# Performance work log

Measured on AMD Instinct MI355X. Metric: run time of the kernel, lower is better.

## Reference

```python
import jax, jax.numpy as jnp
import numpy as np
import math

DIM = 384
NUM_HEADS = 12
WS = 8  # window_size


def setup_inputs() -> dict:
    key = jax.random.key(0)
    k1, k2, k3 = jax.random.split(key, 3)
    B, N, C = 16, 4096, DIM
    x = jax.random.normal(k1, (B, N, C), dtype=jnp.float32)
    W_qkv = jax.random.normal(k2, (C, 3 * C), dtype=jnp.float32) * 0.02
    b_qkv = jnp.zeros((3 * C,), dtype=jnp.float32)
    W_proj = jax.random.normal(k3, (C, C), dtype=jnp.float32) * 0.02
    return {"x": x, "W_qkv": W_qkv, "b_qkv": b_qkv, "W_proj": W_proj}


def window_attention(x, W_qkv, b_qkv, W_proj):
    B, N, C = x.shape
    H = W = int(math.isqrt(N))
    nh = NUM_HEADS
    hd = C // nh
    scale = hd ** (-0.5)
    ws = WS
    pad_h = (ws - H % ws) % ws
    pad_w = (ws - W % ws) % ws
    xg = x.reshape(B, H, W, C)
    if pad_h or pad_w:
        xg = jnp.pad(xg, ((0, 0), (0, pad_h), (0, pad_w), (0, 0)))
    Hp, Wp = H + pad_h, W + pad_w
    nH, nW = Hp // ws, Wp // ws
    # partition into windows: [B, nWin, ws*ws, C]
    xw = xg.reshape(B, nH, ws, nW, ws, C).transpose(0, 1, 3, 2, 4, 5)
    xw = xw.reshape(B, nH * nW, ws * ws, C)
    # qkv projection
    qkv = xw @ W_qkv + b_qkv  # [B, nWin, ws2, 3C]
    qkv = qkv.reshape(B, nH * nW, ws * ws, 3, nh, hd)
    q = qkv[..., 0, :, :].transpose(0, 1, 3, 2, 4)  # [B, nWin, nh, ws2, hd]
    k = qkv[..., 1, :, :].transpose(0, 1, 3, 2, 4)
    v = qkv[..., 2, :, :].transpose(0, 1, 3, 2, 4)
    attn = jnp.einsum('bwhqd,bwhkd->bwhqk', q, k) * scale
    attn = jax.nn.softmax(attn, axis=-1)
    out = jnp.einsum('bwhqk,bwhkd->bwhqd', attn, v)
    out = out.transpose(0, 1, 3, 2, 4).reshape(B, nH * nW, ws * ws, C)
    out = out @ W_proj
    # un-partition windows
    out = out.reshape(B, nH, nW, ws, ws, C).transpose(0, 1, 3, 2, 4, 5)
    out = out.reshape(B, Hp, Wp, C)
    if pad_h or pad_w:
        out = out[:, :H, :W, :]
    return out.reshape(B, H * W, C)


def reference(x, W_qkv, b_qkv, W_proj):
    return window_attention(x, W_qkv, b_qkv, W_proj)
```

## Files before the change

### kernel.cpp

```cpp
#include <hip/hip_runtime.h>
#include <hip/hip_bf16.h>


typedef _Float16 f16;
typedef f16 f16x8 __attribute__((ext_vector_type(8)));
typedef f16 f16x4 __attribute__((ext_vector_type(4)));
typedef float f32x4 __attribute__((ext_vector_type(4)));

#define MFMA_F16(a, b, c) __builtin_amdgcn_mfma_f32_16x16x32_f16((a), (b), (c), 0, 0, 0)

#define AS_G __attribute__((address_space(1)))
#define AS_L __attribute__((address_space(3)))
#define GLOAD_LDS16(gp, lp) \
  __builtin_amdgcn_global_load_lds((const AS_G void*)(gp), (AS_L void*)(lp), 16, 0, 0)
#define WAITVM_(N) asm volatile("s_waitcnt vmcnt(" #N ")" ::: "memory")
#define WAITVM(N) WAITVM_(N)

namespace {
constexpr int kC = 384;
constexpr int kNTok = 4096;
constexpr float kScale = 0.17677669529663687f;
constexpr int kWqPackChunks = 72 * 12 * 64;
constexpr int kWpPackChunks = 24 * 12 * 64;
constexpr size_t kWqPackBytes = (size_t)kWqPackChunks * 16;
constexpr size_t kWpPackBytes = (size_t)kWpPackChunks * 16;
constexpr size_t kQkvWsBytes = (size_t)65536 * 1152 * 2;
constexpr size_t kWsNeed = kWqPackBytes + kWpPackBytes + kQkvWsBytes;
constexpr int kQkvPackChunksFb = 6 * 12 * 12 * 64;
}


__global__ void prep_weights_split(const float* __restrict__ Wqkv,
                                   const float* __restrict__ Wproj,
                                   f16* __restrict__ wq_pack,
                                   f16* __restrict__ wp_pack) {
  int i = blockIdx.x * 256 + threadIdx.x;
  if (i < kWqPackChunks) {
    int lane = i & 63;
    int chunk = i >> 6;
    int ks = chunk % 12;
    int t = chunk / 12;
    int l15 = lane & 15, g = lane >> 4;
    int n3 = t * 16 + l15;
    int k0 = ks * 32 + g * 8;
    f16x8 v;
    #pragma unroll
    for (int j = 0; j < 8; ++j)
      v[j] = (f16)Wqkv[(size_t)(k0 + j) * (3 * kC) + n3];
    *reinterpret_cast<f16x8*>(wq_pack + (size_t)i * 8) = v;
  } else if (i < kWqPackChunks + kWpPackChunks) {
    int p = i - kWqPackChunks;
    int lane = p & 63;
    int chunk = p >> 6;
    int ks = chunk % 12;
    int t = chunk / 12;
    int l15 = lane & 15, g = lane >> 4;
    int n = t * 16 + l15;
    int k0 = ks * 32 + g * 8;
    f16x8 v;
    #pragma unroll
    for (int j = 0; j < 8; ++j)
      v[j] = (f16)Wproj[(size_t)(k0 + j) * kC + n];
    *reinterpret_cast<f16x8*>(wp_pack + (size_t)p * 8) = v;
  }
}

__global__ void prep_x(const float* __restrict__ x, f16* __restrict__ xw) {
  int c = blockIdx.x * 256 + threadIdx.x;
  int lane = c & 63;
  int t = c >> 6;
  int ks = t % 12;
  int mb = t / 12;
  int l15 = lane & 15, g = lane >> 4;
  int m = mb * 16 + l15;
  int b = m >> 12;
  int win = (m >> 6) & 63;
  int tok = m & 63;
  int n = ((win >> 3) * 8 + (tok >> 3)) * 64 + (win & 7) * 8 + (tok & 7);
  const float* src = x + ((size_t)(b << 12) + n) * kC + ks * 32 + g * 8;
  float4 v0 = *reinterpret_cast<const float4*>(src);
  float4 v1 = *reinterpret_cast<const float4*>(src + 4);
  f16x8 h = {(f16)v0.x, (f16)v0.y, (f16)v0.z, (f16)v0.w,
             (f16)v1.x, (f16)v1.y, (f16)v1.z, (f16)v1.w};
  *reinterpret_cast<f16x8*>(xw + (size_t)c * 8) = h;
}

__global__ __launch_bounds__(256, 3) void qkv_gemm2(
    const f16* __restrict__ xw, const float* __restrict__ b_qkv,
    const f16* __restrict__ wq_pack, f16* __restrict__ qkv_ws) {
  __shared__ alignas(1024) char smem[49152];

  const int tid = threadIdx.x;
  const int wid = tid >> 6;
  const int lane = tid & 63;
  const int g = lane >> 4;
  const int l15 = lane & 15;
  const int wm = wid >> 1;
  const int wn = wid & 1;

  int bid = blockIdx.x;
  int wg = (bid & 7) * 576 + (bid >> 3);
  int m_grp = wg / 9;
  int n_grp = wg - m_grp * 9;
  const int mb0 = m_grp * 8;
  const int nb0 = n_grp * 8;

  #define STAGE(KS, BUF)                                                     \
    do {                                                                     \
      const f16* ga0 = xw + (((size_t)(mb0 + wid) * 12 + (KS)) * 64 + lane) * 8;     \
      const f16* ga1 = xw + (((size_t)(mb0 + 4 + wid) * 12 + (KS)) * 64 + lane) * 8; \
      const f16* gb0 =                                                       \
          wq_pack + (((size_t)(nb0 + wid) * 12 + (KS)) * 64 + lane) * 8;     \
      const f16* gb1 =                                                       \
          wq_pack + (((size_t)(nb0 + 4 + wid) * 12 + (KS)) * 64 + lane) * 8; \
      char* la = smem + (BUF) * 16384 + wid * 1024;                          \
      char* lb = smem + (BUF) * 16384 + 8192 + wid * 1024;                   \
      GLOAD_LDS16(ga0, la);                                                  \
      GLOAD_LDS16(ga1, la + 4096);                                           \
      GLOAD_LDS16(gb0, lb);                                                  \
      GLOAD_LDS16(gb1, lb + 4096);                                           \
    } while (0)

  f32x4 acc[4][4];
  #pragma unroll
  for (int mt = 0; mt < 4; ++mt)
    #pragma unroll
    for (int nt = 0; nt < 4; ++nt) acc[mt][nt] = {0.f, 0.f, 0.f, 0.f};

  STAGE(0, 0);
  STAGE(1, 1);
  STAGE(2, 2);
  WAITVM(8);
  __builtin_amdgcn_sched_barrier(0);
  __builtin_amdgcn_s_barrier();

  #define KITER(T, ENDVM)                                                    \
    do {                                                                     \
      constexpr int buf = (T) % 3;                                           \
      f16x8 af[4], bf[4];                                                    \
      _Pragma("unroll") for (int mt = 0; mt < 4; ++mt) af[mt] =              \
          *reinterpret_cast<const f16x8*>(smem + buf * 16384 +               \
                                          (wm * 4 + mt) * 1024 + lane * 16); \
      _Pragma("unroll") for (int nt = 0; nt < 4; ++nt) bf[nt] =              \
          *reinterpret_cast<const f16x8*>(smem + buf * 16384 + 8192 +        \
                                          (wn * 4 + nt) * 1024 + lane * 16); \
      asm volatile("s_waitcnt lgkmcnt(0)" ::: "memory");                     \
      __builtin_amdgcn_sched_barrier(0);                                     \
      __builtin_amdgcn_s_barrier();                                          \
      if ((T) < 9) {                                                         \
        STAGE((T) + 3, buf);                                                 \
      }                                                                      \
      __builtin_amdgcn_s_setprio(1);                                         \
      _Pragma("unroll") for (int mt = 0; mt < 4; ++mt)                       \
          _Pragma("unroll") for (int nt = 0; nt < 4; ++nt) acc[mt][nt] =     \
          MFMA_F16(af[mt], bf[nt], acc[mt][nt]);                             \
      __builtin_amdgcn_s_setprio(0);                                         \
      WAITVM(ENDVM);                                                         \
      __builtin_amdgcn_sched_barrier(0);                                     \
      __builtin_amdgcn_s_barrier();                                          \
    } while (0)

  KITER(0, 8);
  KITER(1, 8);
  KITER(2, 8);
  KITER(3, 8);
  KITER(4, 8);
  KITER(5, 8);
  KITER(6, 8);
  KITER(7, 8);
  KITER(8, 8);
  KITER(9, 4);
  KITER(10, 0);
  KITER(11, 0);
  #undef KITER
  #undef STAGE

  f16* eo = (f16*)smem;
  #pragma unroll
  for (int nt = 0; nt < 4; ++nt) {
    int col128 = wn * 64 + nt * 16 + l15;
    float bias = b_qkv[n_grp * 128 + col128];
    int hsec_loc = wn * 2 + (nt >> 1);
    int d = col128 & 31;
    int sec = (n_grp * 4 + hsec_loc) / 12;
    int base = (wm * 4 + hsec_loc) * 2048;
    #pragma unroll
    for (int mt = 0; mt < 4; ++mt) {
      #pragma unroll
      for (int j = 0; j < 4; ++j) {
        int tok = mt * 16 + g * 4 + j;
        f16 hv = (f16)(acc[mt][nt][j] + bias);
        if (sec == 2)
          eo[base + d * 64 + (tok ^ ((d & 7) << 3))] = hv;
        else
          eo[base + tok * 32 + d] = hv;
      }
    }
  }
  __syncthreads();
  #pragma unroll
  for (int i = 0; i < 8; ++i) {
    int u = tid + i * 256;
    int win_loc = u >> 10;
    int cbl = (u >> 8) & 3;
    int inner = u & 255;
    int cb = n_grp * 4 + cbl;
    int h = cb % 12;
    int sec = cb / 12;
    size_t dst = ((size_t)(m_grp * 2 + win_loc) * 36 + h * 3 + sec) * 2048 +
                 (size_t)inner * 8;
    f16x8 hv;
    if (sec == 2) {
      int d = inner >> 3;
      int t0 = inner & 7;
      hv = *reinterpret_cast<const f16x8*>(
          eo + (win_loc * 4 + cbl) * 2048 + d * 64 + ((t0 * 8) ^ ((d & 7) << 3)));
    } else {
      hv = *reinterpret_cast<const f16x8*>(eo + (size_t)u * 8);
    }
    *reinterpret_cast<f16x8*>(qkv_ws + dst) = hv;
  }
}

__global__ __launch_bounds__(768, 2) void attn_proj2(
    const f16* __restrict__ qkv_ws, const f16* __restrict__ wp_pack,
    float* __restrict__ out) {
  __shared__ alignas(16) f16 ao[64][392];
  __shared__ alignas(16) f16 p_s[12][16][68];

  const int tid = threadIdx.x;
  const int wid = tid >> 6;
  const int lane = tid & 63;
  const int g = lane >> 4;
  const int l15 = lane & 15;

  int blk = (int)blockIdx.x;
  blk = (blk & 7) * 128 + (blk >> 3);
  const int b = blk >> 6;
  const int win = blk & 63;
  const int wh = win >> 3;
  const int ww = win & 7;

  const f32x4 zero4 = {0.f, 0.f, 0.f, 0.f};
  const f16* hb = qkv_ws + ((size_t)(b * 64 + win) * 36 + wid * 3) * 2048;

  f16x8 qf[4], kf[4], vf[2][2];
  #pragma unroll
  for (int mt = 0; mt < 4; ++mt)
    qf[mt] = *reinterpret_cast<const f16x8*>(hb + (mt * 16 + l15) * 32 + g * 8);
  #pragma unroll
  for (int nt = 0; nt < 4; ++nt)
    kf[nt] = *reinterpret_cast<const f16x8*>(hb + 2048 + (nt * 16 + l15) * 32 + g * 8);
  #pragma unroll
  for (int ntd = 0; ntd < 2; ++ntd)
    #pragma unroll
    for (int ks = 0; ks < 2; ++ks)
      vf[ntd][ks] = *reinterpret_cast<const f16x8*>(
          hb + 4096 + (ntd * 16 + l15) * 64 + ks * 32 + g * 8);

  f32x4 sacc[4][4];
  #pragma unroll
  for (int mt = 0; mt < 4; ++mt)
    #pragma unroll
    for (int nt = 0; nt < 4; ++nt) sacc[mt][nt] = zero4;
  #pragma unroll
  for (int mt = 0; mt < 4; ++mt)
    #pragma unroll
    for (int nt = 0; nt < 4; ++nt)
      sacc[mt][nt] = MFMA_F16(qf[mt], kf[nt], sacc[mt][nt]);

  f32x4 oacc[4][2];
  #pragma unroll
  for (int mt = 0; mt < 4; ++mt) {
    oacc[mt][0] = zero4;
    oacc[mt][1] = zero4;
  }
  #pragma unroll
  for (int mt = 0; mt < 4; ++mt) {
    float pv[4][4];
    #pragma unroll
    for (int j = 0; j < 4; ++j) {
      float m = -1e30f;
      #pragma unroll
      for (int nt = 0; nt < 4; ++nt) {
        pv[nt][j] = sacc[mt][nt][j] * kScale;
        m = fmaxf(m, pv[nt][j]);
      }
      m = fmaxf(m, __shfl_xor(m, 1));
      m = fmaxf(m, __shfl_xor(m, 2));
      m = fmaxf(m, __shfl_xor(m, 4));
      m = fmaxf(m, __shfl_xor(m, 8));
      float s = 0.f;
      #pragma unroll
      for (int nt = 0; nt < 4; ++nt) {
        pv[nt][j] = __expf(pv[nt][j] - m);
        s += pv[nt][j];
      }
      s += __shfl_xor(s, 1);
      s += __shfl_xor(s, 2);
      s += __shfl_xor(s, 4);
      s += __shfl_xor(s, 8);
      float inv = 1.0f / s;
      #pragma unroll
      for (int nt = 0; nt < 4; ++nt)
        p_s[wid][g * 4 + j][nt * 16 + l15] = (f16)(pv[nt][j] * inv);
    }
    #pragma unroll
    for (int ks = 0; ks < 2; ++ks) {
      f16x8 pa =
          *reinterpret_cast<const f16x8*>(&p_s[wid][l15][ks * 32 + g * 8]);
      #pragma unroll
      for (int ntd = 0; ntd < 2; ++ntd)
        oacc[mt][ntd] = MFMA_F16(pa, vf[ntd][ks], oacc[mt][ntd]);
    }
    #pragma unroll
    for (int ntd = 0; ntd < 2; ++ntd)
      #pragma unroll
      for (int j = 0; j < 4; ++j)
        ao[mt * 16 + g * 4 + j][wid * 32 + ntd * 16 + l15] =
            (f16)oacc[mt][ntd][j];
  }
  __syncthreads();

  f32x4 pacc[4][2];
  #pragma unroll
  for (int mt = 0; mt < 4; ++mt) {
    pacc[mt][0] = zero4;
    pacc[mt][1] = zero4;
  }
  const f16* pptr[2];
  #pragma unroll
  for (int nt = 0; nt < 2; ++nt) {
    int t = wid * 2 + nt;
    pptr[nt] = wp_pack + ((size_t)(t * 12) * 64 + lane) * 8;
  }
  f16x8 pbf[2][2];
  #pragma unroll
  for (int nt = 0; nt < 2; ++nt)
    pbf[0][nt] = *reinterpret_cast<const f16x8*>(pptr[nt]);

  #pragma unroll
  for (int ks = 0; ks < 12; ++ks) {
    const int cur = ks & 1;
    if (ks < 11) {
      #pragma unroll
      for (int nt = 0; nt < 2; ++nt)
        pbf[cur ^ 1][nt] =
            *reinterpret_cast<const f16x8*>(pptr[nt] + (ks + 1) * 512);
    }
    f16x8 paf[4];
    #pragma unroll
    for (int mt = 0; mt < 4; ++mt)
      paf[mt] = *reinterpret_cast<const f16x8*>(
          &ao[mt * 16 + l15][ks * 32 + g * 8]);
    #pragma unroll
    for (int mt = 0; mt < 4; ++mt)
      #pragma unroll
      for (int nt = 0; nt < 2; ++nt)
        pacc[mt][nt] = MFMA_F16(paf[mt], pbf[cur][nt], pacc[mt][nt]);
  }

  const size_t outbase = (size_t)b * kNTok * kC;
  #pragma unroll
  for (int mt = 0; mt < 4; ++mt) {
    #pragma unroll
    for (int j = 0; j < 4; ++j) {
      int r = mt * 16 + g * 4 + j;
      int n = (wh * 8 + (r >> 3)) * 64 + ww * 8 + (r & 7);
      float* orow = out + outbase + (size_t)n * kC + wid * 32;
      #pragma unroll
      for (int nt = 0; nt < 2; ++nt) orow[nt * 16 + l15] = pacc[mt][nt][j];
    }
  }
}


__global__ void prep_weights_fb(const float* __restrict__ Wqkv,
                                const float* __restrict__ Wproj,
                                f16* __restrict__ wq_pack,
                                f16* __restrict__ wp_pack) {
  int i = blockIdx.x * 256 + threadIdx.x;
  if (i < kQkvPackChunksFb) {
    int lane = i & 63;
    int chunk = i >> 6;
    int ks = chunk % 12;
    int t = (chunk / 12) % 12;
    int hp = chunk / 144;
    int l15 = lane & 15, g = lane >> 4;
    int base = t * 16;
    int hh = base / 96;
    int cc = base - hh * 96;
    int sec = cc >> 5;
    int dbhi = cc & 31;
    int n3 = sec * kC + (2 * hp + hh) * 32 + dbhi + l15;
    int k0 = ks * 32 + g * 8;
    f16x8 v;
    #pragma unroll
    for (int j = 0; j < 8; ++j)
      v[j] = (f16)Wqkv[(size_t)(k0 + j) * (3 * kC) + n3];
    *reinterpret_cast<f16x8*>(wq_pack + (size_t)i * 8) = v;
  } else if (i < kQkvPackChunksFb + kWpPackChunks) {
    int p = i - kQkvPackChunksFb;
    int lane = p & 63;
    int chunk = p >> 6;
    int ks = chunk % 12;
    int t = chunk / 12;
    int l15 = lane & 15, g = lane >> 4;
    int n = t * 16 + l15;
    int k0 = ks * 32 + g * 8;
    f16x8 v;
    #pragma unroll
    for (int j = 0; j < 8; ++j)
      v[j] = (f16)Wproj[(size_t)(k0 + j) * kC + n];
    *reinterpret_cast<f16x8*>(wp_pack + (size_t)p * 8) = v;
  }
}

__global__ __launch_bounds__(512, 2) void win_attn_fused_fb(
    const float* __restrict__ x, const float* __restrict__ b_qkv,
    const f16* __restrict__ wq_pack, const f16* __restrict__ wp_pack,
    float* __restrict__ out) {
  __shared__ alignas(16) f16 xs[64][392];
  __shared__ alignas(16) f16 ao[64][392];
  __shared__ alignas(16) f16 q_s[2][64][40];
  __shared__ alignas(16) f16 k_s[2][64][40];
  __shared__ alignas(16) f16 vT[2][32][72];
  __shared__ alignas(16) f16 p_s[8][16][72];

  const int tid = threadIdx.x;
  const int wid = tid >> 6;
  const int lane = tid & 63;
  const int g = lane >> 4;
  const int l15 = lane & 15;
  const int wm = wid >> 2;
  const int wn = wid & 3;

  const int blk = blockIdx.x;
  const int b = blk >> 6;
  const int win = blk & 63;
  const int wh = win >> 3;
  const int ww = win & 7;

  const f32x4 zero4 = {0.f, 0.f, 0.f, 0.f};

  {
    const float* xb = x + (size_t)b * kNTok * kC;
    #pragma unroll
    for (int it = 0; it < 12; ++it) {
      int idx = tid + it * 512;
      int r = idx / 96;
      int c4 = idx - r * 96;
      int n = (wh * 8 + (r >> 3)) * 64 + ww * 8 + (r & 7);
      float4 v = *reinterpret_cast<const float4*>(xb + (size_t)n * kC + c4 * 4);
      f16x4 hv = {(f16)v.x, (f16)v.y, (f16)v.z, (f16)v.w};
      *reinterpret_cast<f16x4*>(&xs[r][c4 * 4]) = hv;
    }
  }
  __syncthreads();

  for (int hp = 0; hp < 6; ++hp) {
    f32x4 acc[2][3];
    #pragma unroll
    for (int mt = 0; mt < 2; ++mt)
      #pragma unroll
      for (int nt = 0; nt < 3; ++nt) acc[mt][nt] = zero4;

    const f16* bptr[3];
    int secv[3], dbv[3], hhv[3];
    #pragma unroll
    for (int nt = 0; nt < 3; ++nt) {
      int t = wn * 3 + nt;
      int base = t * 16;
      int hh = base / 96;
      int cc = base - hh * 96;
      hhv[nt] = hh;
      secv[nt] = cc >> 5;
      dbv[nt] = cc & 31;
      bptr[nt] = wq_pack + ((size_t)((hp * 12 + t) * 12) * 64 + lane) * 8;
    }

    f16x8 bf[4][3];
    f16x8 af[2][2];
    #pragma unroll
    for (int p = 0; p < 3; ++p)
      #pragma unroll
      for (int nt = 0; nt < 3; ++nt)
        bf[p][nt] = *reinterpret_cast<const f16x8*>(bptr[nt] + p * 512);
    #pragma unroll
    for (int mt = 0; mt < 2; ++mt)
      af[0][mt] = *reinterpret_cast<const f16x8*>(
          &xs[wm * 32 + mt * 16 + l15][g * 8]);

    #pragma unroll
    for (int ks = 0; ks < 12; ++ks) {
      const int cur = ks & 3;
      const int ca = ks & 1;
      if (ks < 9) {
        const int nx = (ks + 3) & 3;
        #pragma unroll
        for (int nt = 0; nt < 3; ++nt)
          bf[nx][nt] =
              *reinterpret_cast<const f16x8*>(bptr[nt] + (ks + 3) * 512);
      }
      if (ks < 11) {
        #pragma unroll
        for (int mt = 0; mt < 2; ++mt)
          af[ca ^ 1][mt] = *reinterpret_cast<const f16x8*>(
              &xs[wm * 32 + mt * 16 + l15][(ks + 1) * 32 + g * 8]);
      }
      #pragma unroll
      for (int mt = 0; mt < 2; ++mt)
        #pragma unroll
        for (int nt = 0; nt < 3; ++nt)
          acc[mt][nt] = MFMA_F16(af[ca][mt], bf[cur][nt], acc[mt][nt]);
    }

    #pragma unroll
    for (int nt = 0; nt < 3; ++nt) {
      int hh = hhv[nt], sec = secv[nt];
      int col = dbv[nt] + l15;
      float bias = b_qkv[sec * kC + (2 * hp + hh) * 32 + col];
      #pragma unroll
      for (int mt = 0; mt < 2; ++mt) {
        #pragma unroll
        for (int j = 0; j < 4; ++j) {
          int r = wm * 32 + mt * 16 + g * 4 + j;
          f16 hv = (f16)(acc[mt][nt][j] + bias);
          if (sec == 0) q_s[hh][r][col] = hv;
          else if (sec == 1) k_s[hh][r][col] = hv;
          else vT[hh][col][r] = hv;
        }
      }
    }
    __syncthreads();

    f32x4 sacc[4];
    #pragma unroll
    for (int nt = 0; nt < 4; ++nt) sacc[nt] = zero4;
    f16x8 qa = *reinterpret_cast<const f16x8*>(&q_s[wm][wn * 16 + l15][g * 8]);
    #pragma unroll
    for (int nt = 0; nt < 4; ++nt) {
      f16x8 kb =
          *reinterpret_cast<const f16x8*>(&k_s[wm][nt * 16 + l15][g * 8]);
      sacc[nt] = MFMA_F16(qa, kb, sacc[nt]);
    }

    float pv[4][4];
    #pragma unroll
    for (int j = 0; j < 4; ++j) {
      float m = -1e30f;
      #pragma unroll
      for (int nt = 0; nt < 4; ++nt) {
        pv[nt][j] = sacc[nt][j] * kScale;
        m = fmaxf(m, pv[nt][j]);
      }
      m = fmaxf(m, __shfl_xor(m, 1));
      m = fmaxf(m, __shfl_xor(m, 2));
      m = fmaxf(m, __shfl_xor(m, 4));
      m = fmaxf(m, __shfl_xor(m, 8));
      float s = 0.f;
      #pragma unroll
      for (int nt = 0; nt < 4; ++nt) {
        pv[nt][j] = __expf(pv[nt][j] - m);
        s += pv[nt][j];
      }
      s += __shfl_xor(s, 1);
      s += __shfl_xor(s, 2);
      s += __shfl_xor(s, 4);
      s += __shfl_xor(s, 8);
      float inv = 1.0f / s;
      #pragma unroll
      for (int nt = 0; nt < 4; ++nt)
        p_s[wid][g * 4 + j][nt * 16 + l15] = (f16)(pv[nt][j] * inv);
    }

    f32x4 oacc[2];
    oacc[0] = zero4;
    oacc[1] = zero4;
    #pragma unroll
    for (int ks = 0; ks < 2; ++ks) {
      f16x8 pa =
          *reinterpret_cast<const f16x8*>(&p_s[wid][l15][ks * 32 + g * 8]);
      #pragma unroll
      for (int nt = 0; nt < 2; ++nt) {
        f16x8 vb = *reinterpret_cast<const f16x8*>(
            &vT[wm][nt * 16 + l15][ks * 32 + g * 8]);
        oacc[nt] = MFMA_F16(pa, vb, oacc[nt]);
      }
    }
    #pragma unroll
    for (int nt = 0; nt < 2; ++nt)
      #pragma unroll
      for (int j = 0; j < 4; ++j)
        ao[wn * 16 + g * 4 + j][(2 * hp + wm) * 32 + nt * 16 + l15] =
            (f16)oacc[nt][j];
    __syncthreads();
  }

  f32x4 pacc[2][6];
  #pragma unroll
  for (int mt = 0; mt < 2; ++mt)
    #pragma unroll
    for (int nt = 0; nt < 6; ++nt) pacc[mt][nt] = zero4;

  const f16* pptr[6];
  #pragma unroll
  for (int nt = 0; nt < 6; ++nt) {
    int t = wn * 6 + nt;
    pptr[nt] = wp_pack + ((size_t)(t * 12) * 64 + lane) * 8;
  }
  f16x8 pbf[3][6];
  f16x8 paf[2][2];
  #pragma unroll
  for (int p = 0; p < 2; ++p)
    #pragma unroll
    for (int nt = 0; nt < 6; ++nt)
      pbf[p][nt] = *reinterpret_cast<const f16x8*>(pptr[nt] + p * 512);
  #pragma unroll
  for (int mt = 0; mt < 2; ++mt)
    paf[0][mt] =
        *reinterpret_cast<const f16x8*>(&ao[wm * 32 + mt * 16 + l15][g * 8]);

  #pragma unroll
  for (int ks = 0; ks < 12; ++ks) {
    const int cur = ks % 3;
    const int ca = ks & 1;
    if (ks < 10) {
      const int nx = (ks + 2) % 3;
      #pragma unroll
      for (int nt = 0; nt < 6; ++nt)
        pbf[nx][nt] =
            *reinterpret_cast<const f16x8*>(pptr[nt] + (ks + 2) * 512);
    }
    if (ks < 11) {
      #pragma unroll
      for (int mt = 0; mt < 2; ++mt)
        paf[ca ^ 1][mt] = *reinterpret_cast<const f16x8*>(
            &ao[wm * 32 + mt * 16 + l15][(ks + 1) * 32 + g * 8]);
    }
    #pragma unroll
    for (int mt = 0; mt < 2; ++mt)
      #pragma unroll
      for (int nt = 0; nt < 6; ++nt)
        pacc[mt][nt] = MFMA_F16(paf[ca][mt], pbf[cur][nt], pacc[mt][nt]);
  }

  const size_t outbase = (size_t)b * kNTok * kC;
  #pragma unroll
  for (int mt = 0; mt < 2; ++mt) {
    #pragma unroll
    for (int j = 0; j < 4; ++j) {
      int r = wm * 32 + mt * 16 + g * 4 + j;
      int n = (wh * 8 + (r >> 3)) * 64 + ww * 8 + (r & 7);
      float* orow = out + outbase + (size_t)n * kC + wn * 96;
      #pragma unroll
      for (int nt = 0; nt < 6; ++nt) orow[nt * 16 + l15] = pacc[mt][nt][j];
    }
  }
}


extern "C" void kernel_launch(void* const* d_in, const int* in_sizes, int n_in,
                              void* d_out, int out_size, void* d_ws,
                              size_t ws_size, hipStream_t stream) {
  const float* x = (const float*)d_in[0];
  const float* Wqkv = (const float*)d_in[1];
  const float* bqkv = (const float*)d_in[2];
  const float* Wproj = (const float*)d_in[3];
  float* out = (float*)d_out;

  if (ws_size >= kWsNeed) {
    f16* wq_pack = (f16*)d_ws;
    f16* wp_pack = (f16*)((char*)d_ws + kWqPackBytes);
    f16* qkv_ws = (f16*)((char*)d_ws + kWqPackBytes + kWpPackBytes);
    f16* xw = (f16*)d_out;

    int prep_threads = kWqPackChunks + kWpPackChunks;
    hipLaunchKernelGGL(prep_weights_split, dim3((prep_threads + 255) / 256),
                       dim3(256), 0, stream, Wqkv, Wproj, wq_pack, wp_pack);
    hipLaunchKernelGGL(prep_x, dim3(12288), dim3(256), 0, stream, x, xw);
    hipLaunchKernelGGL(qkv_gemm2, dim3(4608), dim3(256), 0, stream, xw, bqkv,
                       wq_pack, qkv_ws);
    hipLaunchKernelGGL(attn_proj2, dim3(16 * 64), dim3(768), 0, stream, qkv_ws,
                       wp_pack, out);
  } else {
    f16* wq_pack = (f16*)d_ws;
    f16* wp_pack = (f16*)((char*)d_ws + (size_t)kQkvPackChunksFb * 16);
    int prep_threads = kQkvPackChunksFb + kWpPackChunks;
    hipLaunchKernelGGL(prep_weights_fb, dim3((prep_threads + 255) / 256),
                       dim3(256), 0, stream, Wqkv, Wproj, wq_pack, wp_pack);
    hipLaunchKernelGGL(win_attn_fused_fb, dim3(16 * 64), dim3(512), 0, stream,
                       x, bqkv, wq_pack, wp_pack, out);
  }
}
```

Baseline: 184.1 us.

## Fuse x conversion into QKV GEMM and process two windows per attention block

Removes the separate prep_x kernel. The QKV GEMM now loads fp32 x rows directly through registers, converts them to f16 and writes them to LDS in a software pipeline alongside the async weight loads. The attention kernel now handles two windows per block and prefetches the second window's QKV during the first window's compute. The softmax is reorganized to reduce across the transposed score layout with fewer shuffles. This saves an extra round-trip of the f16 x copy through memory, but the GEMM re-reads fp32 x nine times (once per N group) and the register-staged A path adds register pressure.

```diff
diff --git a/kernel.cpp b/kernel.cpp
--- a/kernel.cpp
+++ b/kernel.cpp
@@ -65,28 +65,8 @@
   }
 }
 
-__global__ void prep_x(const float* __restrict__ x, f16* __restrict__ xw) {
-  int c = blockIdx.x * 256 + threadIdx.x;
-  int lane = c & 63;
-  int t = c >> 6;
-  int ks = t % 12;
-  int mb = t / 12;
-  int l15 = lane & 15, g = lane >> 4;
-  int m = mb * 16 + l15;
-  int b = m >> 12;
-  int win = (m >> 6) & 63;
-  int tok = m & 63;
-  int n = ((win >> 3) * 8 + (tok >> 3)) * 64 + (win & 7) * 8 + (tok & 7);
-  const float* src = x + ((size_t)(b << 12) + n) * kC + ks * 32 + g * 8;
-  float4 v0 = *reinterpret_cast<const float4*>(src);
-  float4 v1 = *reinterpret_cast<const float4*>(src + 4);
-  f16x8 h = {(f16)v0.x, (f16)v0.y, (f16)v0.z, (f16)v0.w,
-             (f16)v1.x, (f16)v1.y, (f16)v1.z, (f16)v1.w};
-  *reinterpret_cast<f16x8*>(xw + (size_t)c * 8) = h;
-}
-
-__global__ __launch_bounds__(256, 3) void qkv_gemm2(
-    const f16* __restrict__ xw, const float* __restrict__ b_qkv,
+__global__ __launch_bounds__(256, 3) void qkv_gemm3(
+    const float* __restrict__ x, const float* __restrict__ b_qkv,
     const f16* __restrict__ wq_pack, f16* __restrict__ qkv_ws) {
   __shared__ alignas(1024) char smem[49152];
 
@@ -104,37 +84,73 @@
   int n_grp = wg - m_grp * 9;
   const int mb0 = m_grp * 8;
   const int nb0 = n_grp * 8;
-
-  #define STAGE(KS, BUF)                                                     \
+  (void)mb0;
+
+  const int r = tid >> 1;
+  const int s = tid & 1;
+  const int rl = r & 15;
+  const float4* xrow4;
+  {
+    int m = m_grp * 128 + r;
+    int b = m >> 12, win = (m >> 6) & 63, tok = m & 63;
+    int n = ((win >> 3) * 8 + (tok >> 3)) * 64 + (win & 7) * 8 + (tok & 7);
+    xrow4 = reinterpret_cast<const float4*>(
+        x + ((size_t)(b << 12) + n) * kC + s * 16);
+  }
+
+  #define BSTAGE(KS, BUF)                                                    \
     do {                                                                     \
-      const f16* ga0 = xw + (((size_t)(mb0 + wid) * 12 + (KS)) * 64 + lane) * 8;     \
-      const f16* ga1 = xw + (((size_t)(mb0 + 4 + wid) * 12 + (KS)) * 64 + lane) * 8; \
       const f16* gb0 =                                                       \
           wq_pack + (((size_t)(nb0 + wid) * 12 + (KS)) * 64 + lane) * 8;     \
       const f16* gb1 =                                                       \
           wq_pack + (((size_t)(nb0 + 4 + wid) * 12 + (KS)) * 64 + lane) * 8; \
-      char* la = smem + (BUF) * 16384 + wid * 1024;                          \
       char* lb = smem + (BUF) * 16384 + 8192 + wid * 1024;                   \
-      GLOAD_LDS16(ga0, la);                                                  \
-      GLOAD_LDS16(ga1, la + 4096);                                           \
       GLOAD_LDS16(gb0, lb);                                                  \
       GLOAD_LDS16(gb1, lb + 4096);                                           \
     } while (0)
 
+  #define ALOAD(KS, R)                                                       \
+    do {                                                                     \
+      R[0] = xrow4[(KS) * 8 + 0];                                            \
+      R[1] = xrow4[(KS) * 8 + 1];                                            \
+      R[2] = xrow4[(KS) * 8 + 2];                                            \
+      R[3] = xrow4[(KS) * 8 + 3];                                            \
+    } while (0)
+
+  #define AWRITE(R, BUF)                                                     \
+    do {                                                                     \
+      f16x8 h0 = {(f16)R[0].x, (f16)R[0].y, (f16)R[0].z, (f16)R[0].w,        \
+                  (f16)R[1].x, (f16)R[1].y, (f16)R[1].z, (f16)R[1].w};       \
+      f16x8 h1 = {(f16)R[2].x, (f16)R[2].y, (f16)R[2].z, (f16)R[2].w,        \
+                  (f16)R[3].x, (f16)R[3].y, (f16)R[3].z, (f16)R[3].w};       \
+      char* ab = smem + (BUF) * 16384 + (r >> 4) * 1024;                     \
+      *reinterpret_cast<f16x8*>(ab + (s * 32 + rl) * 16) = h0;               \
+      *reinterpret_cast<f16x8*>(ab + (s * 32 + 16 + rl) * 16) = h1;          \
+    } while (0)
+
   f32x4 acc[4][4];
   #pragma unroll
   for (int mt = 0; mt < 4; ++mt)
     #pragma unroll
     for (int nt = 0; nt < 4; ++nt) acc[mt][nt] = {0.f, 0.f, 0.f, 0.f};
 
-  STAGE(0, 0);
-  STAGE(1, 1);
-  STAGE(2, 2);
-  WAITVM(8);
+  float4 RA[4], RB[4];
+  BSTAGE(0, 0);
+  BSTAGE(1, 1);
+  BSTAGE(2, 2);
+  ALOAD(0, RA);
+  ALOAD(1, RB);
+  WAITVM(0);
+  __builtin_amdgcn_sched_barrier(0);
+  AWRITE(RA, 0);
+  AWRITE(RB, 1);
+  ALOAD(2, RA);
+  ALOAD(3, RB);
+  asm volatile("s_waitcnt lgkmcnt(0)" ::: "memory");
   __builtin_amdgcn_sched_barrier(0);
   __builtin_amdgcn_s_barrier();
 
-  #define KITER(T, ENDVM)                                                    \
+  #define KITER(T, TOPW)                                                     \
     do {                                                                     \
       constexpr int buf = (T) % 3;                                           \
       f16x8 af[4], bf[4];                                                    \
@@ -147,33 +163,40 @@
       asm volatile("s_waitcnt lgkmcnt(0)" ::: "memory");                     \
       __builtin_amdgcn_sched_barrier(0);                                     \
       __builtin_amdgcn_s_barrier();                                          \
-      if ((T) < 9) {                                                         \
-        STAGE((T) + 3, buf);                                                 \
+      TOPW;                                                                  \
+      __builtin_amdgcn_sched_barrier(0);                                     \
+      if ((T) <= 9) {                                                        \
+        if ((T) & 1) { AWRITE(RB, ((T) + 2) % 3); }                          \
+        else { AWRITE(RA, ((T) + 2) % 3); }                                  \
+      }                                                                      \
+      if ((T) <= 8) { BSTAGE((T) + 3, buf); }                                \
+      if ((T) <= 7) {                                                        \
+        if ((T) & 1) { ALOAD((T) + 4, RB); } else { ALOAD((T) + 4, RA); }    \
       }                                                                      \
       __builtin_amdgcn_s_setprio(1);                                         \
       _Pragma("unroll") for (int mt = 0; mt < 4; ++mt)                       \
           _Pragma("unroll") for (int nt = 0; nt < 4; ++nt) acc[mt][nt] =     \
           MFMA_F16(af[mt], bf[nt], acc[mt][nt]);                             \
       __builtin_amdgcn_s_setprio(0);                                         \
-      WAITVM(ENDVM);                                                         \
-      __builtin_amdgcn_sched_barrier(0);                                     \
       __builtin_amdgcn_s_barrier();                                          \
     } while (0)
 
-  KITER(0, 8);
-  KITER(1, 8);
-  KITER(2, 8);
-  KITER(3, 8);
-  KITER(4, 8);
-  KITER(5, 8);
-  KITER(6, 8);
-  KITER(7, 8);
-  KITER(8, 8);
-  KITER(9, 4);
-  KITER(10, 0);
-  KITER(11, 0);
+  KITER(0, WAITVM(4));
+  KITER(1, WAITVM(6));
+  KITER(2, WAITVM(6));
+  KITER(3, WAITVM(6));
+  KITER(4, WAITVM(6));
+  KITER(5, WAITVM(6));
+  KITER(6, WAITVM(6));
+  KITER(7, WAITVM(6));
+  KITER(8, WAITVM(6));
+  KITER(9, WAITVM(2));
+  KITER(10, WAITVM(0));
+  KITER(11, WAITVM(0));
   #undef KITER
-  #undef STAGE
+  #undef BSTAGE
+  #undef ALOAD
+  #undef AWRITE
 
   f16* eo = (f16*)smem;
   #pragma unroll
@@ -222,7 +245,133 @@
   }
 }
 
-__global__ __launch_bounds__(768, 2) void attn_proj2(
+__device__ __forceinline__ void load_qkv(const f16* __restrict__ hb,
+                                         f16x8 (&qf)[4], f16x8 (&kf)[4],
+                                         f16x8 (&vf)[2][2], int g, int l15) {
+  #pragma unroll
+  for (int mt = 0; mt < 4; ++mt)
+    qf[mt] = *reinterpret_cast<const f16x8*>(hb + (mt * 16 + l15) * 32 + g * 8);
+  #pragma unroll
+  for (int nt = 0; nt < 4; ++nt)
+    kf[nt] = *reinterpret_cast<const f16x8*>(hb + 2048 + (nt * 16 + l15) * 32 +
+                                             g * 8);
+  #pragma unroll
+  for (int nd = 0; nd < 2; ++nd)
+    #pragma unroll
+    for (int ks = 0; ks < 2; ++ks)
+      vf[nd][ks] = *reinterpret_cast<const f16x8*>(
+          hb + 4096 + (nd * 16 + l15) * 64 + ks * 32 + g * 8);
+}
+
+__device__ __forceinline__ void attn_one(const f16x8 (&qf)[4],
+                                         const f16x8 (&kf)[4],
+                                         const f16x8 (&vf)[2][2],
+                                         f16 (&ao)[64][392], f16 (&ps)[16][68],
+                                         int wid, int g, int l15) {
+  const f32x4 zero4 = {0.f, 0.f, 0.f, 0.f};
+  #pragma unroll
+  for (int mt = 0; mt < 4; ++mt) {
+    f32x4 sw0 = MFMA_F16(kf[0], qf[mt], zero4);
+    f32x4 sw1 = MFMA_F16(kf[1], qf[mt], zero4);
+    f32x4 sw2 = MFMA_F16(kf[2], qf[mt], zero4);
+    f32x4 sw3 = MFMA_F16(kf[3], qf[mt], zero4);
+    float p[16];
+    #pragma unroll
+    for (int j = 0; j < 4; ++j) {
+      p[j] = sw0[j] * kScale;
+      p[4 + j] = sw1[j] * kScale;
+      p[8 + j] = sw2[j] * kScale;
+      p[12 + j] = sw3[j] * kScale;
+    }
+    float m0 = fmaxf(fmaxf(p[0], p[1]), fmaxf(p[2], p[3]));
+    float m1 = fmaxf(fmaxf(p[4], p[5]), fmaxf(p[6], p[7]));
+    float m2 = fmaxf(fmaxf(p[8], p[9]), fmaxf(p[10], p[11]));
+    float m3 = fmaxf(fmaxf(p[12], p[13]), fmaxf(p[14], p[15]));
+    float mx = fmaxf(fmaxf(m0, m1), fmaxf(m2, m3));
+    mx = fmaxf(mx, __shfl_xor(mx, 16));
+    mx = fmaxf(mx, __shfl_xor(mx, 32));
+    #pragma unroll
+    for (int i = 0; i < 16; ++i) p[i] = __expf(p[i] - mx);
+    float s01 = (p[0] + p[1]) + (p[2] + p[3]);
+    float s23 = (p[4] + p[5]) + (p[6] + p[7]);
+    float s45 = (p[8] + p[9]) + (p[10] + p[11]);
+    float s67 = (p[12] + p[13]) + (p[14] + p[15]);
+    float s = (s01 + s23) + (s45 + s67);
+    s += __shfl_xor(s, 16);
+    s += __shfl_xor(s, 32);
+    float inv = __builtin_amdgcn_rcpf(s);
+    #pragma unroll
+    for (int nt = 0; nt < 4; ++nt) {
+      f16x4 h = {(f16)(p[nt * 4] * inv), (f16)(p[nt * 4 + 1] * inv),
+                 (f16)(p[nt * 4 + 2] * inv), (f16)(p[nt * 4 + 3] * inv)};
+      *reinterpret_cast<f16x4*>(&ps[l15][nt * 16 + g * 4]) = h;
+    }
+    f32x4 o0 = zero4, o1 = zero4;
+    #pragma unroll
+    for (int ks = 0; ks < 2; ++ks) {
+      f16x8 pa = *reinterpret_cast<const f16x8*>(&ps[l15][ks * 32 + g * 8]);
+      o0 = MFMA_F16(pa, vf[0][ks], o0);
+      o1 = MFMA_F16(pa, vf[1][ks], o1);
+    }
+    #pragma unroll
+    for (int j = 0; j < 4; ++j) {
+      ao[mt * 16 + g * 4 + j][wid * 32 + l15] = (f16)o0[j];
+      ao[mt * 16 + g * 4 + j][wid * 32 + 16 + l15] = (f16)o1[j];
+    }
+  }
+}
+
+__device__ __forceinline__ void proj_store(const f16 (&ao)[64][392],
+                                           const f16* __restrict__ wp_pack,
+                                           float* __restrict__ out, int b,
+                                           int win, int wid, int g, int l15,
+                                           int lane) {
+  const f32x4 zero4 = {0.f, 0.f, 0.f, 0.f};
+  const int wh = win >> 3, ww = win & 7;
+  f32x4 pacc[4][2];
+  #pragma unroll
+  for (int mt = 0; mt < 4; ++mt) {
+    pacc[mt][0] = zero4;
+    pacc[mt][1] = zero4;
+  }
+  const f16* pp0 = wp_pack + ((size_t)((wid * 2) * 12) * 64 + lane) * 8;
+  const f16* pp1 = wp_pack + ((size_t)((wid * 2 + 1) * 12) * 64 + lane) * 8;
+  f16x8 pb0[2], pb1[2];
+  pb0[0] = *reinterpret_cast<const f16x8*>(pp0);
+  pb1[0] = *reinterpret_cast<const f16x8*>(pp1);
+  #pragma unroll
+  for (int ks = 0; ks < 12; ++ks) {
+    const int cur = ks & 1;
+    if (ks < 11) {
+      pb0[cur ^ 1] = *reinterpret_cast<const f16x8*>(pp0 + (ks + 1) * 512);
+      pb1[cur ^ 1] = *reinterpret_cast<const f16x8*>(pp1 + (ks + 1) * 512);
+    }
+    f16x8 paf[4];
+    #pragma unroll
+    for (int mt = 0; mt < 4; ++mt)
+      paf[mt] = *reinterpret_cast<const f16x8*>(
+          &ao[mt * 16 + l15][ks * 32 + g * 8]);
+    #pragma unroll
+    for (int mt = 0; mt < 4; ++mt) {
+      pacc[mt][0] = MFMA_F16(paf[mt], pb0[cur], pacc[mt][0]);
+      pacc[mt][1] = MFMA_F16(paf[mt], pb1[cur], pacc[mt][1]);
+    }
+  }
+  const size_t outbase = (size_t)b * kNTok * kC;
+  #pragma unroll
+  for (int mt = 0; mt < 4; ++mt) {
+    #pragma unroll
+    for (int j = 0; j < 4; ++j) {
+      int rr = mt * 16 + g * 4 + j;
+      int n = (wh * 8 + (rr >> 3)) * 64 + ww * 8 + (rr & 7);
+      float* orow = out + outbase + (size_t)n * kC + wid * 32;
+      orow[l15] = pacc[mt][0][j];
+      orow[16 + l15] = pacc[mt][1][j];
+    }
+  }
+}
+
+__global__ __launch_bounds__(768, 3) void attn_proj3(
     const f16* __restrict__ qkv_ws, const f16* __restrict__ wp_pack,
     float* __restrict__ out) {
   __shared__ alignas(16) f16 ao[64][392];
@@ -234,144 +383,27 @@
   const int g = lane >> 4;
   const int l15 = lane & 15;
 
-  int blk = (int)blockIdx.x;
-  blk = (blk & 7) * 128 + (blk >> 3);
-  const int b = blk >> 6;
-  const int win = blk & 63;
-  const int wh = win >> 3;
-  const int ww = win & 7;
-
-  const f32x4 zero4 = {0.f, 0.f, 0.f, 0.f};
-  const f16* hb = qkv_ws + ((size_t)(b * 64 + win) * 36 + wid * 3) * 2048;
-
-  f16x8 qf[4], kf[4], vf[2][2];
-  #pragma unroll
-  for (int mt = 0; mt < 4; ++mt)
-    qf[mt] = *reinterpret_cast<const f16x8*>(hb + (mt * 16 + l15) * 32 + g * 8);
-  #pragma unroll
-  for (int nt = 0; nt < 4; ++nt)
-    kf[nt] = *reinterpret_cast<const f16x8*>(hb + 2048 + (nt * 16 + l15) * 32 + g * 8);
-  #pragma unroll
-  for (int ntd = 0; ntd < 2; ++ntd)
-    #pragma unroll
-    for (int ks = 0; ks < 2; ++ks)
-      vf[ntd][ks] = *reinterpret_cast<const f16x8*>(
-          hb + 4096 + (ntd * 16 + l15) * 64 + ks * 32 + g * 8);
-
-  f32x4 sacc[4][4];
-  #pragma unroll
-  for (int mt = 0; mt < 4; ++mt)
-    #pragma unroll
-    for (int nt = 0; nt < 4; ++nt) sacc[mt][nt] = zero4;
-  #pragma unroll
-  for (int mt = 0; mt < 4; ++mt)
-    #pragma unroll
-    for (int nt = 0; nt < 4; ++nt)
-      sacc[mt][nt] = MFMA_F16(qf[mt], kf[nt], sacc[mt][nt]);
-
-  f32x4 oacc[4][2];
-  #pragma unroll
-  for (int mt = 0; mt < 4; ++mt) {
-    oacc[mt][0] = zero4;
-    oacc[mt][1] = zero4;
-  }
-  #pragma unroll
-  for (int mt = 0; mt < 4; ++mt) {
-    float pv[4][4];
-    #pragma unroll
-    for (int j = 0; j < 4; ++j) {
-      float m = -1e30f;
-      #pragma unroll
-      for (int nt = 0; nt < 4; ++nt) {
-        pv[nt][j] = sacc[mt][nt][j] * kScale;
-        m = fmaxf(m, pv[nt][j]);
-      }
-      m = fmaxf(m, __shfl_xor(m, 1));
-      m = fmaxf(m, __shfl_xor(m, 2));
-      m = fmaxf(m, __shfl_xor(m, 4));
-      m = fmaxf(m, __shfl_xor(m, 8));
-      float s = 0.f;
-      #pragma unroll
-      for (int nt = 0; nt < 4; ++nt) {
-        pv[nt][j] = __expf(pv[nt][j] - m);
-        s += pv[nt][j];
-      }
-      s += __shfl_xor(s, 1);
-      s += __shfl_xor(s, 2);
-      s += __shfl_xor(s, 4);
-      s += __shfl_xor(s, 8);
-      float inv = 1.0f / s;
-      #pragma unroll
-      for (int nt = 0; nt < 4; ++nt)
-        p_s[wid][g * 4 + j][nt * 16 + l15] = (f16)(pv[nt][j] * inv);
-    }
-    #pragma unroll
-    for (int ks = 0; ks < 2; ++ks) {
-      f16x8 pa =
-          *reinterpret_cast<const f16x8*>(&p_s[wid][l15][ks * 32 + g * 8]);
-      #pragma unroll
-      for (int ntd = 0; ntd < 2; ++ntd)
-        oacc[mt][ntd] = MFMA_F16(pa, vf[ntd][ks], oacc[mt][ntd]);
-    }
-    #pragma unroll
-    for (int ntd = 0; ntd < 2; ++ntd)
-      #pragma unroll
-      for (int j = 0; j < 4; ++j)
-        ao[mt * 16 + g * 4 + j][wid * 32 + ntd * 16 + l15] =
-            (f16)oacc[mt][ntd][j];
-  }
+  int bid = (int)blockIdx.x;
+  int w2 = (bid & 7) * 64 + (bid >> 3);
+  const int b = w2 >> 5;
+  const int win0 = (w2 & 31) * 2;
+  const int win1 = win0 + 1;
+
+  const f16* hb0 = qkv_ws + ((size_t)(b * 64 + win0) * 36 + wid * 3) * 2048;
+  const f16* hb1 = hb0 + 36 * 2048;
+
+  f16x8 qA[4], kA[4], vA[2][2], qB[4], kB[4], vB[2][2];
+  load_qkv(hb0, qA, kA, vA, g, l15);
+  __builtin_amdgcn_sched_barrier(0);
+  attn_one(qA, kA, vA, ao, p_s[wid], wid, g, l15);
+  load_qkv(hb1, qB, kB, vB, g, l15);
+  __builtin_amdgcn_sched_barrier(0);
   __syncthreads();
-
-  f32x4 pacc[4][2];
-  #pragma unroll
-  for (int mt = 0; mt < 4; ++mt) {
-    pacc[mt][0] = zero4;
-    pacc[mt][1] = zero4;
-  }
-  const f16* pptr[2];
-  #pragma unroll
-  for (int nt = 0; nt < 2; ++nt) {
-    int t = wid * 2 + nt;
-    pptr[nt] = wp_pack + ((size_t)(t * 12) * 64 + lane) * 8;
-  }
-  f16x8 pbf[2][2];
-  #pragma unroll
-  for (int nt = 0; nt < 2; ++nt)
-    pbf[0][nt] = *reinterpret_cast<const f16x8*>(pptr[nt]);
-
-  #pragma unroll
-  for (int ks = 0; ks < 12; ++ks) {
-    const int cur = ks & 1;
-    if (ks < 11) {
-      #pragma unroll
-      for (int nt = 0; nt < 2; ++nt)
-        pbf[cur ^ 1][nt] =
-            *reinterpret_cast<const f16x8*>(pptr[nt] + (ks + 1) * 512);
-    }
-    f16x8 paf[4];
-    #pragma unroll
-    for (int mt = 0; mt < 4; ++mt)
-      paf[mt] = *reinterpret_cast<const f16x8*>(
-          &ao[mt * 16 + l15][ks * 32 + g * 8]);
-    #pragma unroll
-    for (int mt = 0; mt < 4; ++mt)
-      #pragma unroll
-      for (int nt = 0; nt < 2; ++nt)
-        pacc[mt][nt] = MFMA_F16(paf[mt], pbf[cur][nt], pacc[mt][nt]);
-  }
-
-  const size_t outbase = (size_t)b * kNTok * kC;
-  #pragma unroll
-  for (int mt = 0; mt < 4; ++mt) {
-    #pragma unroll
-    for (int j = 0; j < 4; ++j) {
-      int r = mt * 16 + g * 4 + j;
-      int n = (wh * 8 + (r >> 3)) * 64 + ww * 8 + (r & 7);
-      float* orow = out + outbase + (size_t)n * kC + wid * 32;
-      #pragma unroll
-      for (int nt = 0; nt < 2; ++nt) orow[nt * 16 + l15] = pacc[mt][nt][j];
-    }
-  }
+  proj_store(ao, wp_pack, out, b, win0, wid, g, l15, lane);
+  __syncthreads();
+  attn_one(qB, kB, vB, ao, p_s[wid], wid, g, l15);
+  __syncthreads();
+  proj_store(ao, wp_pack, out, b, win1, wid, g, l15, lane);
 }
 
 
@@ -673,15 +705,13 @@
     f16* wq_pack = (f16*)d_ws;
     f16* wp_pack = (f16*)((char*)d_ws + kWqPackBytes);
     f16* qkv_ws = (f16*)((char*)d_ws + kWqPackBytes + kWpPackBytes);
-    f16* xw = (f16*)d_out;
 
     int prep_threads = kWqPackChunks + kWpPackChunks;
     hipLaunchKernelGGL(prep_weights_split, dim3((prep_threads + 255) / 256),
                        dim3(256), 0, stream, Wqkv, Wproj, wq_pack, wp_pack);
-    hipLaunchKernelGGL(prep_x, dim3(12288), dim3(256), 0, stream, x, xw);
-    hipLaunchKernelGGL(qkv_gemm2, dim3(4608), dim3(256), 0, stream, xw, bqkv,
+    hipLaunchKernelGGL(qkv_gemm3, dim3(4608), dim3(256), 0, stream, x, bqkv,
                        wq_pack, qkv_ws);
-    hipLaunchKernelGGL(attn_proj2, dim3(16 * 64), dim3(768), 0, stream, qkv_ws,
+    hipLaunchKernelGGL(attn_proj3, dim3(512), dim3(768), 0, stream, qkv_ws,
                        wp_pack, out);
   } else {
     f16* wq_pack = (f16*)d_ws;
```

Result: slower. 210.9 us (+14.6%).
